# Optimization experiments

Hardware: AMD Instinct MI355X
Metric: run time of the kernel (lower is better)

The kernel has to match this reference:

```python
import jax, jax.numpy as jnp
import numpy as np

N0, N1, N2 = 16000, 12000, 6000
K0, K1 = 10, 5
H, OUT = 256, 128
VOCABS = [50000, 1000, 200]
EDIMS = [64, 32, 32]
EIN = sum(EDIMS)  # 128 input to fc_input


def setup_inputs() -> dict:
    key = jax.random.key(0)
    ks = jax.random.split(key, 40)
    inp = {}
    cols = [jax.random.randint(ks[i], (N0, 1), 0, VOCABS[i]) for i in range(3)]
    inp['x'] = jnp.concatenate(cols, axis=1)
    inp['idx_sim0'] = jax.random.randint(ks[3], (N1, K0), 0, N0)
    inp['idx_cor0'] = jax.random.randint(ks[4], (N1, K0), 0, N0)
    inp['idx_sim1'] = jax.random.randint(ks[5], (N2, K1), 0, N1)
    inp['idx_cor1'] = jax.random.randint(ks[6], (N2, K1), 0, N1)
    k = 7
    for m in ['sim', 'cor']:
        for i in range(3):
            inp[f'emb{i}_{m}'] = jax.random.normal(ks[k], (VOCABS[i], EDIMS[i]), jnp.float32) * 0.02; k += 1
        inp[f'Win_{m}'] = jax.random.normal(ks[k], (EIN, H), jnp.float32) * (1.0 / np.sqrt(EIN)); k += 1
        inp[f'bin_{m}'] = jnp.zeros((H,), jnp.float32)
        inp[f'Wout_{m}'] = jax.random.normal(ks[k], (H, OUT), jnp.float32) * (1.0 / np.sqrt(H)); k += 1
        inp[f'bout_{m}'] = jnp.zeros((OUT,), jnp.float32)
    inp['Ws2c'] = jax.random.normal(ks[k], (OUT, OUT), jnp.float32) * (1.0 / np.sqrt(OUT)); k += 1
    inp['Wc2s'] = jax.random.normal(ks[k], (OUT, OUT), jnp.float32) * (1.0 / np.sqrt(OUT)); k += 1
    inp['a1'] = jnp.array([0.3], jnp.float32)
    inp['a2'] = jnp.array([0.25], jnp.float32)
    inp['b2'] = jnp.array([0.2], jnp.float32)
    return inp


def _coattention(D, Q):
    # D, Q: [N, K, H]
    L = jnp.einsum('nkh,nmh->nkm', D, Q)          # [N, K, K]
    AC = jax.nn.softmax(L, axis=-1)
    AS = jax.nn.softmax(jnp.swapaxes(L, 1, 2), axis=-1)
    CQ = jnp.einsum('nkm,nmh->nkh', AC, Q)        # [N, K, H]
    CD = jnp.einsum('nkm,nmh->nkh', AS, jnp.concatenate([D, CQ], axis=-1))  # [N, K, 2H]
    return jnp.concatenate([Q, CD], axis=-1)       # [N, K, 3H]


def _coagg(feat, idx_sim, idx_cor, mode, n_dst):
    # gather neighbor features per dst node (feat_src[in_edges_id])
    if mode == 'cor':
        D, Q = feat[idx_sim], feat[idx_cor]
    else:
        D, Q = feat[idx_cor], feat[idx_sim]
    h = _coattention(D, Q)                         # [n_dst, K, 3H]
    n, k, f = h.shape
    # AvgPool1d(kernel=3, stride=3) over feature axis -> [n_dst, K, H]
    pooled = h.reshape(n, k, f // 3, 3).mean(axis=-1)
    neigh = pooled.mean(axis=1)                    # mean over neighbors -> [n_dst, H]
    return feat[:n_dst] + neigh


def _branch(x, e0, e1, e2, Win, bin_, Wout, bout, i_s0, i_c0, i_s1, i_c1, mode):
    e = jnp.concatenate([e0[x[:, 0]], e1[x[:, 1]], e2[x[:, 2]]], axis=1)  # [N0, 128]
    h = e @ Win + bin_                             # [N0, H]
    h = jax.nn.relu(_coagg(h, i_s0, i_c0, mode, N1))
    h = _coagg(h, i_s1, i_c1, mode, N2)
    return h @ Wout + bout                         # [N2, OUT]


def reference(x, idx_sim0, idx_cor0, idx_sim1, idx_cor1,
              emb0_sim, emb1_sim, emb2_sim, Win_sim, bin_sim, Wout_sim, bout_sim,
              emb0_cor, emb1_cor, emb2_cor, Win_cor, bin_cor, Wout_cor, bout_cor,
              Ws2c, Wc2s, a1, a2, b2):
    sim = _branch(x, emb0_sim, emb1_sim, emb2_sim, Win_sim, bin_sim, Wout_sim, bout_sim,
                  idx_sim0, idx_cor0, idx_sim1, idx_cor1, 'sim')
    cor = _branch(x, emb0_cor, emb1_cor, emb2_cor, Win_cor, bin_cor, Wout_cor, bout_cor,
                  idx_sim0, idx_cor0, idx_sim1, idx_cor1, 'cor')
    # SemanticIntegration
    z1sim = (1 - a1) * sim + a1 * (cor @ Wc2s)
    z1cor = (1 - a1) * cor + a1 * (sim @ Ws2c)
    z2sim = (1 - a2 - b2) * sim + a2 * (cor @ Wc2s) + b2 * (z1cor @ Wc2s)
    z2cor = (1 - a2 - b2) * cor + a2 * (sim @ Ws2c) + b2 * (z1sim @ Ws2c)
    return jnp.stack([z2sim, z2cor])               # [2, N2, OUT]
```

## Files before the change

### kernel.cpp

```cpp
#include <hip/hip_runtime.h>

#define CH 256

template <int CTRL>
__device__ __forceinline__ float dppAdd(float v) {
    const int m = __builtin_amdgcn_update_dpp(0, __builtin_bit_cast(int, v), CTRL, 0xf, 0xf, true);
    return v + __builtin_bit_cast(float, m);
}

#define OPAQUE4(v) asm volatile("" : "+v"((v).x), "+v"((v).y), "+v"((v).z), "+v"((v).w))

__device__ __forceinline__ unsigned short f2bf(float f) {
    unsigned int x = __builtin_bit_cast(unsigned int, f);
    return (unsigned short)((x + 0x7fffu + ((x >> 16) & 1u)) >> 16);
}
__device__ __forceinline__ float bf2f(unsigned short u) {
    return __builtin_bit_cast(float, ((unsigned int)u) << 16);
}

__global__ __launch_bounds__(256) void embed_fc2_kernel(
    const int* __restrict__ x,
    const float* __restrict__ e0a, const float* __restrict__ e1a, const float* __restrict__ e2a,
    const float* __restrict__ Wina, const float* __restrict__ bina, unsigned short* __restrict__ h0a,
    const float* __restrict__ e0b, const float* __restrict__ e1b, const float* __restrict__ e2b,
    const float* __restrict__ Winb, const float* __restrict__ binb, unsigned short* __restrict__ h0b,
    const int blocksPer)
{
    __shared__ __align__(16) float eT[128][32];
    int bid = blockIdx.x;
    const float *e0, *e1, *e2, *Win, *bin;
    unsigned short* h0;
    if (bid < blocksPer) { e0 = e0a; e1 = e1a; e2 = e2a; Win = Wina; bin = bina; h0 = h0a; }
    else { bid -= blocksPer; e0 = e0b; e1 = e1b; e2 = e2b; Win = Winb; bin = binb; h0 = h0b; }

    const int row0 = bid * 32;
    const int t = threadIdx.x;
    const int w = t >> 6, l = t & 63;
    const int r = l & 31;
    const int kcBase = 2 * w + (l >> 5);

#pragma unroll
    for (int j = 0; j < 4; ++j) {
        const int kc = kcBase + 8 * j;
        const int k0 = kc * 4;
        const int row = row0 + r;
        float4 v;
        if (kc < 16)      v = *(const float4*)(e0 + (size_t)x[row * 3 + 0] * 64 + k0);
        else if (kc < 24) v = *(const float4*)(e1 + (size_t)x[row * 3 + 1] * 32 + (k0 - 64));
        else              v = *(const float4*)(e2 + (size_t)x[row * 3 + 2] * 32 + (k0 - 96));
        eT[k0 + 0][r] = v.x; eT[k0 + 1][r] = v.y; eT[k0 + 2][r] = v.z; eT[k0 + 3][r] = v.w;
    }
    __syncthreads();

    const float4 bb = *(const float4*)(bin + l * 4);
    float acc[8][4];
#pragma unroll
    for (int rr = 0; rr < 8; ++rr) {
        acc[rr][0] = bb.x; acc[rr][1] = bb.y; acc[rr][2] = bb.z; acc[rr][3] = bb.w;
    }
#pragma unroll 4
    for (int k = 0; k < 128; ++k) {
        const float4 wv = *(const float4*)(Win + (size_t)k * 256 + l * 4);
        const float4 ea = *(const float4*)&eT[k][w * 8];
        const float4 eb = *(const float4*)&eT[k][w * 8 + 4];
        const float ev[8] = {ea.x, ea.y, ea.z, ea.w, eb.x, eb.y, eb.z, eb.w};
#pragma unroll
        for (int rr = 0; rr < 8; ++rr) {
            acc[rr][0] += ev[rr] * wv.x; acc[rr][1] += ev[rr] * wv.y;
            acc[rr][2] += ev[rr] * wv.z; acc[rr][3] += ev[rr] * wv.w;
        }
    }
#pragma unroll
    for (int rr = 0; rr < 8; ++rr) {
        ushort4 o;
        o.x = f2bf(acc[rr][0]); o.y = f2bf(acc[rr][1]);
        o.z = f2bf(acc[rr][2]); o.w = f2bf(acc[rr][3]);
        *(ushort4*)(h0 + (size_t)(row0 + w * 8 + rr) * 256 + l * 4) = o;
    }
}

template <int KD, int MODE>
__global__ __launch_bounds__(128) void gemm16_kernel(
    const float* __restrict__ ina, const float* __restrict__ Wa,
    const float* __restrict__ auxa, const float* __restrict__ aux2a, float* __restrict__ oa,
    const float* __restrict__ inb, const float* __restrict__ Wb,
    const float* __restrict__ auxb, const float* __restrict__ aux2b, float* __restrict__ ob,
    const int blocksPer, const int nRows,
    const float* __restrict__ a1p, const float* __restrict__ a2p, const float* __restrict__ b2p)
{
    __shared__ __align__(16) float inT[KD][16];
    int bid = blockIdx.x;
    const float *in, *W, *aux, *aux2; float* outp;
    if (bid < blocksPer) { in = ina; W = Wa; aux = auxa; aux2 = aux2a; outp = oa; }
    else { bid -= blocksPer; in = inb; W = Wb; aux = auxb; aux2 = aux2b; outp = ob; }

    const int row0 = bid * 16;
    const int t = threadIdx.x;
    const int row = t & 15;
    const int kc0 = t >> 4;

#pragma unroll
    for (int j = 0; j < KD / 32; ++j) {
        const int kc = kc0 + 8 * j;
        const int k0 = kc * 4;
        int r = row0 + row;
        if (r >= nRows) r = nRows - 1;
        const float4 v = *(const float4*)(in + (size_t)r * KD + k0);
        inT[k0 + 0][row] = v.x; inT[k0 + 1][row] = v.y;
        inT[k0 + 2][row] = v.z; inT[k0 + 3][row] = v.w;
    }
    __syncthreads();

    const int w = t >> 6, l = t & 63;
    const int rg = w * 2 + (l >> 5);
    const int r0 = rg * 4;
    const int cc0 = (l & 31) * 4;

    float acc[4][4];
    if constexpr (MODE == 0) {
        const float4 bb = *(const float4*)(aux + cc0);
#pragma unroll
        for (int rr = 0; rr < 4; ++rr) {
            acc[rr][0] = bb.x; acc[rr][1] = bb.y; acc[rr][2] = bb.z; acc[rr][3] = bb.w;
        }
    } else {
#pragma unroll
        for (int rr = 0; rr < 4; ++rr) acc[rr][0] = acc[rr][1] = acc[rr][2] = acc[rr][3] = 0.f;
    }

#pragma unroll 4
    for (int k = 0; k < KD; ++k) {
        const float4 wv = *(const float4*)(W + (size_t)k * 128 + cc0);
        const float4 ea = *(const float4*)&inT[k][r0];
        const float ev[4] = {ea.x, ea.y, ea.z, ea.w};
#pragma unroll
        for (int rr = 0; rr < 4; ++rr) {
            acc[rr][0] += ev[rr] * wv.x; acc[rr][1] += ev[rr] * wv.y;
            acc[rr][2] += ev[rr] * wv.z; acc[rr][3] += ev[rr] * wv.w;
        }
    }

    float c0 = 0.f, c1 = 0.f, c2 = 0.f;
    if constexpr (MODE == 1) {
        const float a1 = *a1p, a2 = *a2p, b2 = *b2p;
        c0 = 1.f - a2 - b2;
        c1 = a2 + b2 * (1.f - a1);
        c2 = b2 * a1;
    }

#pragma unroll
    for (int rr = 0; rr < 4; ++rr) {
        const int r = row0 + r0 + rr;
        if (r < nRows) {
            float4 o = make_float4(acc[rr][0], acc[rr][1], acc[rr][2], acc[rr][3]);
            if constexpr (MODE == 1) {
                const size_t idx = (size_t)r * 128 + cc0;
                const float4 b1v = *(const float4*)(aux + idx);
                const float4 b2v = *(const float4*)(aux2 + idx);
                o.x = c0 * b1v.x + c1 * b2v.x + c2 * o.x;
                o.y = c0 * b1v.y + c1 * b2v.y + c2 * o.y;
                o.z = c0 * b1v.z + c1 * b2v.z + c2 * o.z;
                o.w = c0 * b1v.w + c1 * b2v.w + c2 * o.w;
            }
            *(float4*)(outp + (size_t)r * 128 + cc0) = o;
        }
    }
}

template <int K, bool BF16IN, bool BF16OUT>
__global__ __launch_bounds__(256, 2) void coagg_kernel(
    const void* __restrict__ fa, const int* __restrict__ iDa, const int* __restrict__ iQa,
    void* __restrict__ oa,
    const void* __restrict__ fb, const int* __restrict__ iDb, const int* __restrict__ iQb,
    void* __restrict__ ob,
    const int nPer, const int relu)
{
    __shared__ float sL[4][K][K];
    __shared__ float sAC[4][K][K];
    __shared__ float sAS[4][K][K];
    __shared__ float sw_[4][K], su_[4][K];
    __shared__ __align__(16) float sHsum[4][768];

    const int t = threadIdx.x;
    const int wv = t >> 6, lane = t & 63;
    int n = blockIdx.x * 4 + wv;

    const void* feat; const int* idxD; const int* idxQ; void* outp;
    if (n < nPer) { feat = fa; idxD = iDa; idxQ = iQa; outp = oa; }
    else { n -= nPer; feat = fb; idxD = iDb; idxQ = iQb; outp = ob; }

    float4 d[K], q[K], resid;
    if constexpr (BF16IN) {
        const unsigned short* fpu = (const unsigned short*)feat;
#pragma unroll
        for (int k = 0; k < K; ++k) {
            const int rD = idxD[n * K + k];
            const int rQ = idxQ[n * K + k];
            const ushort4 ud = *(const ushort4*)(fpu + (size_t)rD * 256 + lane * 4);
            const ushort4 uq = *(const ushort4*)(fpu + (size_t)rQ * 256 + lane * 4);
            d[k] = make_float4(bf2f(ud.x), bf2f(ud.y), bf2f(ud.z), bf2f(ud.w));
            q[k] = make_float4(bf2f(uq.x), bf2f(uq.y), bf2f(uq.z), bf2f(uq.w));
        }
        const ushort4 ur = *(const ushort4*)(fpu + (size_t)n * 256 + lane * 4);
        resid = make_float4(bf2f(ur.x), bf2f(ur.y), bf2f(ur.z), bf2f(ur.w));
    } else {
        const float4* fp = (const float4*)feat;
#pragma unroll
        for (int k = 0; k < K; ++k) {
            const int rD = idxD[n * K + k];
            const int rQ = idxQ[n * K + k];
            d[k] = fp[(size_t)rD * 64 + lane];
            q[k] = fp[(size_t)rQ * 64 + lane];
        }
        resid = fp[(size_t)n * 64 + lane];
    }
#pragma unroll
    for (int k = 0; k < K; ++k) { OPAQUE4(d[k]); OPAQUE4(q[k]); }

#pragma unroll
    for (int k = 0; k < K; ++k) {
        const float4 dd = d[k];
#pragma unroll
        for (int m0 = 0; m0 < K; m0 += 4) {
            const float4 q0 = q[m0];
            float s0 = dd.x * q0.x + dd.y * q0.y + dd.z * q0.z + dd.w * q0.w;
            float s1 = 0.f, s2 = 0.f, s3 = 0.f;
            if (m0 + 1 < K) {
                const float4 qq = q[(m0 + 1 < K) ? m0 + 1 : 0];
                s1 = dd.x * qq.x + dd.y * qq.y + dd.z * qq.z + dd.w * qq.w;
            }
            if (m0 + 2 < K) {
                const float4 qq = q[(m0 + 2 < K) ? m0 + 2 : 0];
                s2 = dd.x * qq.x + dd.y * qq.y + dd.z * qq.z + dd.w * qq.w;
            }
            if (m0 + 3 < K) {
                const float4 qq = q[(m0 + 3 < K) ? m0 + 3 : 0];
                s3 = dd.x * qq.x + dd.y * qq.y + dd.z * qq.z + dd.w * qq.w;
            }
            asm volatile("v_permlane32_swap_b32 %0, %1" : "+v"(s0), "+v"(s1));
            float a = s0 + s1;
            asm volatile("v_permlane32_swap_b32 %0, %1" : "+v"(s2), "+v"(s3));
            float b = s2 + s3;
            asm volatile("v_permlane16_swap_b32 %0, %1" : "+v"(a), "+v"(b));
            float r = a + b;
            r = dppAdd<0x111>(r);
            r = dppAdd<0x112>(r);
            r = dppAdd<0x114>(r);
            r = dppAdd<0x118>(r);
            const int rowid = lane >> 4;
            const int mm = m0 + (((rowid & 1) << 1) | (rowid >> 1));
            if ((lane & 15) == 15 && mm < K) sL[wv][k][mm] = r;
        }
    }

    if (lane < K) {
        float e_[K], mx = -1e30f;
#pragma unroll
        for (int m = 0; m < K; ++m) mx = fmaxf(mx, sL[wv][lane][m]);
        float ssum = 0.f;
#pragma unroll
        for (int m = 0; m < K; ++m) { e_[m] = __expf(sL[wv][lane][m] - mx); ssum += e_[m]; }
        const float inv = 1.f / ssum;
#pragma unroll
        for (int m = 0; m < K; ++m) sAC[wv][lane][m] = e_[m] * inv;
    }
    {
        const int c = lane - 16;
        if (c >= 0 && c < K) {
            float e_[K], mx = -1e30f;
#pragma unroll
            for (int m = 0; m < K; ++m) mx = fmaxf(mx, sL[wv][m][c]);
            float ssum = 0.f;
#pragma unroll
            for (int m = 0; m < K; ++m) { e_[m] = __expf(sL[wv][m][c] - mx); ssum += e_[m]; }
            const float inv = 1.f / ssum;
#pragma unroll
            for (int m = 0; m < K; ++m) sAS[wv][c][m] = e_[m] * inv;
        }
    }
    {
        const int m2 = lane - 32;
        if (m2 >= 0 && m2 < K) {
            float s = 0.f;
#pragma unroll
            for (int k2 = 0; k2 < K; ++k2) s += sAS[wv][k2][m2];
            sw_[wv][m2] = s;
        }
    }
    {
        const int j2 = lane - 48;
        if (j2 >= 0 && j2 < K) {
            float s = 0.f;
#pragma unroll
            for (int m = 0; m < K; ++m) s += sw_[wv][m] * sAC[wv][m][j2];
            su_[wv][j2] = s;
        }
    }

    float4 h0v = make_float4(0.f, 0.f, 0.f, 0.f);
    float4 h1v = make_float4(0.f, 0.f, 0.f, 0.f);
    float4 h2v = make_float4(0.f, 0.f, 0.f, 0.f);
#pragma unroll
    for (int kx = 0; kx < K; ++kx) {
        const float wk = sw_[wv][kx];
        const float uk = su_[wv][kx];
        const float4 qq = q[kx];
        const float4 dd = d[kx];
        h0v.x += qq.x;      h0v.y += qq.y;      h0v.z += qq.z;      h0v.w += qq.w;
        h1v.x += wk * dd.x; h1v.y += wk * dd.y; h1v.z += wk * dd.z; h1v.w += wk * dd.w;
        h2v.x += uk * qq.x; h2v.y += uk * qq.y; h2v.z += uk * qq.z; h2v.w += uk * qq.w;
    }
    ((float4*)&sHsum[wv][0])[lane]       = h0v;
    ((float4*)&sHsum[wv][0])[64 + lane]  = h1v;
    ((float4*)&sHsum[wv][0])[128 + lane] = h2v;

    float ov[4];
#pragma unroll
    for (int i = 0; i < 4; ++i) {
        const int f = lane * 4 + i;
        ov[i] = (sHsum[wv][3 * f] + sHsum[wv][3 * f + 1] + sHsum[wv][3 * f + 2])
                * (1.0f / (3.0f * K));
    }
    float4 o = make_float4(resid.x + ov[0], resid.y + ov[1],
                           resid.z + ov[2], resid.w + ov[3]);
    if (relu) {
        o.x = fmaxf(o.x, 0.f); o.y = fmaxf(o.y, 0.f);
        o.z = fmaxf(o.z, 0.f); o.w = fmaxf(o.w, 0.f);
    }
    if constexpr (BF16OUT) {
        ushort4 ou;
        ou.x = f2bf(o.x); ou.y = f2bf(o.y); ou.z = f2bf(o.z); ou.w = f2bf(o.w);
        *(ushort4*)((unsigned short*)outp + (size_t)n * 256 + lane * 4) = ou;
    } else {
        ((float4*)outp)[(size_t)n * 64 + lane] = o;
    }
}

extern "C" void kernel_launch(void* const* d_in, const int* in_sizes, int n_in,
                              void* d_out, int out_size, void* d_ws, size_t ws_size,
                              hipStream_t stream)
{
    const int* x        = (const int*)d_in[0];
    const int* idx_sim0 = (const int*)d_in[1];
    const int* idx_cor0 = (const int*)d_in[2];
    const int* idx_sim1 = (const int*)d_in[3];
    const int* idx_cor1 = (const int*)d_in[4];
    const float* e0s  = (const float*)d_in[5];
    const float* e1s  = (const float*)d_in[6];
    const float* e2s  = (const float*)d_in[7];
    const float* Wins = (const float*)d_in[8];
    const float* bins = (const float*)d_in[9];
    const float* Wouts= (const float*)d_in[10];
    const float* bouts= (const float*)d_in[11];
    const float* e0c  = (const float*)d_in[12];
    const float* e1c  = (const float*)d_in[13];
    const float* e2c  = (const float*)d_in[14];
    const float* Winc = (const float*)d_in[15];
    const float* binc = (const float*)d_in[16];
    const float* Woutc= (const float*)d_in[17];
    const float* boutc= (const float*)d_in[18];
    const float* Ws2c = (const float*)d_in[19];
    const float* Wc2s = (const float*)d_in[20];
    const float* a1 = (const float*)d_in[21];
    const float* a2 = (const float*)d_in[22];
    const float* b2 = (const float*)d_in[23];

    float* outSim = (float*)d_out;
    float* outCor = outSim + 6000 * 128;

    float* ws = (float*)d_ws;
    const size_t needMerged = (size_t)(2 * 16000 * 256 + 2 * 12000 * 256 + 2 * 6000 * 256 + 4 * 6000 * 128) * 4;
    const bool merged = ws_size >= needMerged;

    const int fcBlocks = 6000 / 16;

    if (merged) {
        unsigned short* A0 = (unsigned short*)ws;
        unsigned short* A1 = (unsigned short*)(ws + 16000 * 256);
        unsigned short* B0 = (unsigned short*)(ws + 2 * 16000 * 256);
        unsigned short* B1 = (unsigned short*)(ws + 2 * 16000 * 256 + 12000 * 256);
        float* C0 = ws + 2 * 16000 * 256 + 2 * 12000 * 256;
        float* C1 = C0 + 6000 * 256;
        float* simO = C1 + 6000 * 256;
        float* corO = simO + 6000 * 128;
        float* P    = corO + 6000 * 128;
        float* S    = P + 6000 * 128;

        embed_fc2_kernel<<<1000, 256, 0, stream>>>(x,
            e0s, e1s, e2s, Wins, bins, A0,
            e0c, e1c, e2c, Winc, binc, A1, 500);
        coagg_kernel<10, true, true><<<6000, 256, 0, stream>>>(
            A0, idx_cor0, idx_sim0, B0,
            A1, idx_sim0, idx_cor0, B1, 12000, 1);
        coagg_kernel<5, true, false><<<3000, 256, 0, stream>>>(
            B0, idx_cor1, idx_sim1, C0,
            B1, idx_sim1, idx_cor1, C1, 6000, 0);
        gemm16_kernel<256, 0><<<2 * fcBlocks, 128, 0, stream>>>(
            C0, Wouts, bouts, nullptr, simO,
            C1, Woutc, boutc, nullptr, corO, fcBlocks, 6000, a1, a2, b2);
        gemm16_kernel<128, 2><<<2 * fcBlocks, 128, 0, stream>>>(
            corO, Wc2s, nullptr, nullptr, P,
            simO, Ws2c, nullptr, nullptr, S, fcBlocks, 6000, a1, a2, b2);
        gemm16_kernel<128, 1><<<2 * fcBlocks, 128, 0, stream>>>(
            S, Wc2s, simO, P, outSim,
            P, Ws2c, corO, S, outCor, fcBlocks, 6000, a1, a2, b2);
    } else {
        unsigned short* A = (unsigned short*)ws;
        unsigned short* B = (unsigned short*)(ws + 16000 * 256);
        float* C = ws + 16000 * 256 + 12000 * 256;
        float* simO = C + 6000 * 256;
        float* corO = simO + 6000 * 128;
        float* P    = corO + 6000 * 128;
        float* S    = P + 6000 * 128;

        for (int b = 0; b < 2; ++b) {
            const float* e0   = (b == 0) ? e0s : e0c;
            const float* e1   = (b == 0) ? e1s : e1c;
            const float* e2   = (b == 0) ? e2s : e2c;
            const float* Win  = (b == 0) ? Wins : Winc;
            const float* bin  = (b == 0) ? bins : binc;
            const float* Wout = (b == 0) ? Wouts : Woutc;
            const float* bout = (b == 0) ? bouts : boutc;
            const int* iD0 = (b == 0) ? idx_cor0 : idx_sim0;
            const int* iQ0 = (b == 0) ? idx_sim0 : idx_cor0;
            const int* iD1 = (b == 0) ? idx_cor1 : idx_sim1;
            const int* iQ1 = (b == 0) ? idx_sim1 : idx_cor1;
            float* branchOut = (b == 0) ? simO : corO;

            embed_fc2_kernel<<<500, 256, 0, stream>>>(x,
                e0, e1, e2, Win, bin, A,
                e0, e1, e2, Win, bin, A, 500);
            coagg_kernel<10, true, true><<<3000, 256, 0, stream>>>(
                A, iD0, iQ0, B, A, iD0, iQ0, B, 12000, 1);
            coagg_kernel<5, true, false><<<1500, 256, 0, stream>>>(
                B, iD1, iQ1, C, B, iD1, iQ1, C, 6000, 0);
            gemm16_kernel<256, 0><<<fcBlocks, 128, 0, stream>>>(
                C, Wout, bout, nullptr, branchOut,
                C, Wout, bout, nullptr, branchOut, fcBlocks, 6000, a1, a2, b2);
        }
        gemm16_kernel<128, 2><<<2 * fcBlocks, 128, 0, stream>>>(
            corO, Wc2s, nullptr, nullptr, P,
            simO, Ws2c, nullptr, nullptr, S, fcBlocks, 6000, a1, a2, b2);
        gemm16_kernel<128, 1><<<2 * fcBlocks, 128, 0, stream>>>(
            S, Wc2s, simO, P, outSim,
            P, Ws2c, corO, S, outCor, fcBlocks, 6000, a1, a2, b2);
    }
}
```

Measured before the change: 150.5 us.

## Compute coattention score matrix with bf16 MFMA instead of VALU dot products

Replaces the per-wave VALU dot products and permlane/DPP reductions that build the K×K score matrix with a 16x16x32 bf16 MFMA accumulation over the 256-wide feature dimension. Each lane loads its own D/Q neighbor rows in 16-byte chunks directly from the gathered bf16 features. The float4 D/Q register arrays are dropped, so neighbor rows and the residual are re-read from global memory in the aggregation phase. This cuts ALU work and register pressure but doubles gather traffic, which may hit cache.

```diff
diff --git a/kernel.cpp b/kernel.cpp
--- a/kernel.cpp
+++ b/kernel.cpp
@@ -2,13 +2,8 @@
 
 #define CH 256
 
-template <int CTRL>
-__device__ __forceinline__ float dppAdd(float v) {
-    const int m = __builtin_amdgcn_update_dpp(0, __builtin_bit_cast(int, v), CTRL, 0xf, 0xf, true);
-    return v + __builtin_bit_cast(float, m);
-}
-
-#define OPAQUE4(v) asm volatile("" : "+v"((v).x), "+v"((v).y), "+v"((v).z), "+v"((v).w))
+typedef __attribute__((ext_vector_type(8))) short bf16x8;
+typedef __attribute__((ext_vector_type(4))) float f32x4;
 
 __device__ __forceinline__ unsigned short f2bf(float f) {
     unsigned int x = __builtin_bit_cast(unsigned int, f);
@@ -167,11 +162,11 @@
     }
 }
 
-template <int K, bool BF16IN, bool BF16OUT>
+template <int K, bool BF16OUT>
 __global__ __launch_bounds__(256, 2) void coagg_kernel(
-    const void* __restrict__ fa, const int* __restrict__ iDa, const int* __restrict__ iQa,
+    const unsigned short* __restrict__ fa, const int* __restrict__ iDa, const int* __restrict__ iQa,
     void* __restrict__ oa,
-    const void* __restrict__ fb, const int* __restrict__ iDb, const int* __restrict__ iQb,
+    const unsigned short* __restrict__ fb, const int* __restrict__ iDb, const int* __restrict__ iQb,
     void* __restrict__ ob,
     const int nPer, const int relu)
 {
@@ -185,72 +180,30 @@
     const int wv = t >> 6, lane = t & 63;
     int n = blockIdx.x * 4 + wv;
 
-    const void* feat; const int* idxD; const int* idxQ; void* outp;
+    const unsigned short* feat; const int* idxD; const int* idxQ; void* outp;
     if (n < nPer) { feat = fa; idxD = iDa; idxQ = iQa; outp = oa; }
     else { n -= nPer; feat = fb; idxD = iDb; idxQ = iQb; outp = ob; }
 
-    float4 d[K], q[K], resid;
-    if constexpr (BF16IN) {
-        const unsigned short* fpu = (const unsigned short*)feat;
-#pragma unroll
-        for (int k = 0; k < K; ++k) {
-            const int rD = idxD[n * K + k];
-            const int rQ = idxQ[n * K + k];
-            const ushort4 ud = *(const ushort4*)(fpu + (size_t)rD * 256 + lane * 4);
-            const ushort4 uq = *(const ushort4*)(fpu + (size_t)rQ * 256 + lane * 4);
-            d[k] = make_float4(bf2f(ud.x), bf2f(ud.y), bf2f(ud.z), bf2f(ud.w));
-            q[k] = make_float4(bf2f(uq.x), bf2f(uq.y), bf2f(uq.z), bf2f(uq.w));
-        }
-        const ushort4 ur = *(const ushort4*)(fpu + (size_t)n * 256 + lane * 4);
-        resid = make_float4(bf2f(ur.x), bf2f(ur.y), bf2f(ur.z), bf2f(ur.w));
-    } else {
-        const float4* fp = (const float4*)feat;
-#pragma unroll
-        for (int k = 0; k < K; ++k) {
-            const int rD = idxD[n * K + k];
-            const int rQ = idxQ[n * K + k];
-            d[k] = fp[(size_t)rD * 64 + lane];
-            q[k] = fp[(size_t)rQ * 64 + lane];
-        }
-        resid = fp[(size_t)n * 64 + lane];
-    }
-#pragma unroll
-    for (int k = 0; k < K; ++k) { OPAQUE4(d[k]); OPAQUE4(q[k]); }
-
-#pragma unroll
-    for (int k = 0; k < K; ++k) {
-        const float4 dd = d[k];
-#pragma unroll
-        for (int m0 = 0; m0 < K; m0 += 4) {
-            const float4 q0 = q[m0];
-            float s0 = dd.x * q0.x + dd.y * q0.y + dd.z * q0.z + dd.w * q0.w;
-            float s1 = 0.f, s2 = 0.f, s3 = 0.f;
-            if (m0 + 1 < K) {
-                const float4 qq = q[(m0 + 1 < K) ? m0 + 1 : 0];
-                s1 = dd.x * qq.x + dd.y * qq.y + dd.z * qq.z + dd.w * qq.w;
-            }
-            if (m0 + 2 < K) {
-                const float4 qq = q[(m0 + 2 < K) ? m0 + 2 : 0];
-                s2 = dd.x * qq.x + dd.y * qq.y + dd.z * qq.z + dd.w * qq.w;
-            }
-            if (m0 + 3 < K) {
-                const float4 qq = q[(m0 + 3 < K) ? m0 + 3 : 0];
-                s3 = dd.x * qq.x + dd.y * qq.y + dd.z * qq.z + dd.w * qq.w;
-            }
-            asm volatile("v_permlane32_swap_b32 %0, %1" : "+v"(s0), "+v"(s1));
-            float a = s0 + s1;
-            asm volatile("v_permlane32_swap_b32 %0, %1" : "+v"(s2), "+v"(s3));
-            float b = s2 + s3;
-            asm volatile("v_permlane16_swap_b32 %0, %1" : "+v"(a), "+v"(b));
-            float r = a + b;
-            r = dppAdd<0x111>(r);
-            r = dppAdd<0x112>(r);
-            r = dppAdd<0x114>(r);
-            r = dppAdd<0x118>(r);
-            const int rowid = lane >> 4;
-            const int mm = m0 + (((rowid & 1) << 1) | (rowid >> 1));
-            if ((lane & 15) == 15 && mm < K) sL[wv][k][mm] = r;
-        }
+    const int r16 = lane & 15;
+    const int kh  = lane >> 4;
+    const int rCl = (r16 < K) ? r16 : 0;
+    const int rowD = idxD[n * K + rCl];
+    const int rowQ = idxQ[n * K + rCl];
+    const uint4* fd = (const uint4*)(feat + (size_t)rowD * 256);
+    const uint4* fq = (const uint4*)(feat + (size_t)rowQ * 256);
+
+    f32x4 acc = {0.f, 0.f, 0.f, 0.f};
+#pragma unroll
+    for (int s = 0; s < 8; ++s) {
+        const uint4 av = fd[s * 4 + kh];
+        const uint4 bv = fq[s * 4 + kh];
+        acc = __builtin_amdgcn_mfma_f32_16x16x32_bf16(
+            __builtin_bit_cast(bf16x8, av), __builtin_bit_cast(bf16x8, bv), acc, 0, 0, 0);
+    }
+#pragma unroll
+    for (int reg = 0; reg < 4; ++reg) {
+        const int row = kh * 4 + reg;
+        if (row < K && r16 < K) sL[wv][row][r16] = acc[reg];
     }
 
     if (lane < K) {
@@ -304,8 +257,10 @@
     for (int kx = 0; kx < K; ++kx) {
         const float wk = sw_[wv][kx];
         const float uk = su_[wv][kx];
-        const float4 qq = q[kx];
-        const float4 dd = d[kx];
+        const ushort4 ud = *(const ushort4*)(feat + (size_t)idxD[n * K + kx] * 256 + lane * 4);
+        const ushort4 uq = *(const ushort4*)(feat + (size_t)idxQ[n * K + kx] * 256 + lane * 4);
+        const float4 dd = make_float4(bf2f(ud.x), bf2f(ud.y), bf2f(ud.z), bf2f(ud.w));
+        const float4 qq = make_float4(bf2f(uq.x), bf2f(uq.y), bf2f(uq.z), bf2f(uq.w));
         h0v.x += qq.x;      h0v.y += qq.y;      h0v.z += qq.z;      h0v.w += qq.w;
         h1v.x += wk * dd.x; h1v.y += wk * dd.y; h1v.z += wk * dd.z; h1v.w += wk * dd.w;
         h2v.x += uk * qq.x; h2v.y += uk * qq.y; h2v.z += uk * qq.z; h2v.w += uk * qq.w;
@@ -314,6 +269,8 @@
     ((float4*)&sHsum[wv][0])[64 + lane]  = h1v;
     ((float4*)&sHsum[wv][0])[128 + lane] = h2v;
 
+    const ushort4 ur = *(const ushort4*)(feat + (size_t)n * 256 + lane * 4);
+    const float4 resid = make_float4(bf2f(ur.x), bf2f(ur.y), bf2f(ur.z), bf2f(ur.w));
     float ov[4];
 #pragma unroll
     for (int i = 0; i < 4; ++i) {
@@ -389,10 +346,10 @@
         embed_fc2_kernel<<<1000, 256, 0, stream>>>(x,
             e0s, e1s, e2s, Wins, bins, A0,
             e0c, e1c, e2c, Winc, binc, A1, 500);
-        coagg_kernel<10, true, true><<<6000, 256, 0, stream>>>(
+        coagg_kernel<10, true><<<6000, 256, 0, stream>>>(
             A0, idx_cor0, idx_sim0, B0,
             A1, idx_sim0, idx_cor0, B1, 12000, 1);
-        coagg_kernel<5, true, false><<<3000, 256, 0, stream>>>(
+        coagg_kernel<5, false><<<3000, 256, 0, stream>>>(
             B0, idx_cor1, idx_sim1, C0,
             B1, idx_sim1, idx_cor1, C1, 6000, 0);
         gemm16_kernel<256, 0><<<2 * fcBlocks, 128, 0, stream>>>(
@@ -430,9 +387,9 @@
             embed_fc2_kernel<<<500, 256, 0, stream>>>(x,
                 e0, e1, e2, Win, bin, A,
                 e0, e1, e2, Win, bin, A, 500);
-            coagg_kernel<10, true, true><<<3000, 256, 0, stream>>>(
+            coagg_kernel<10, true><<<3000, 256, 0, stream>>>(
                 A, iD0, iQ0, B, A, iD0, iQ0, B, 12000, 1);
-            coagg_kernel<5, true, false><<<1500, 256, 0, stream>>>(
+            coagg_kernel<5, false><<<1500, 256, 0, stream>>>(
                 B, iD1, iQ1, C, B, iD1, iQ1, C, 6000, 0);
             gemm16_kernel<256, 0><<<fcBlocks, 128, 0, stream>>>(
                 C, Wout, bout, nullptr, branchOut,
```

Result: slower. 164.7 us (+9.4%).
